# Kernel tuning notes

Hardware: AMD Instinct MI355X
Metric: run time of the kernel (lower is better)

## Reference

```python
import jax, jax.numpy as jnp
import numpy as np

M, N, K, T, BATCH = 1024, 128, 256, 10, 8192
LAMBD = 1.0


def setup_inputs() -> dict:
    key = jax.random.key(0)
    ks = jax.random.split(key, 4)
    y = jax.random.normal(ks[0], (BATCH, 2, N), dtype=jnp.float32)
    # xavier_normal scales, matching nn.init.xavier_normal_
    W = jax.random.normal(ks[1], (2, N, K), dtype=jnp.float32) * np.float32(np.sqrt(2.0 / (N + K)))
    WX = jax.random.normal(ks[2], (2, K, N), dtype=jnp.float32) * np.float32(np.sqrt(2.0 / (K + N)))
    E0 = jax.random.normal(ks[3], (2, M, K), dtype=jnp.float32) * np.float32(np.sqrt(2.0 / (M + K)))
    etas = jnp.full((T + 1, 1, 1), 1e-4, dtype=jnp.float32)   # original init 1e-4*ones
    gammas = jnp.ones((T + 1, 1, 1), dtype=jnp.float32)       # original init ones
    return {"y": y, "W": W, "WX": WX, "E0": E0, "etas": etas, "gammas": gammas}


def cmatmul(A, X):
    # complex matmul in 2-channel real form: A (2,p,q), X (2,q,B) -> (2,p,B)
    re = A[0] @ X[0] - A[1] @ X[1]
    im = A[0] @ X[1] + A[1] @ X[0]
    return jnp.stack([re, im])


def softshrink(z, lambd):
    return jnp.sign(z) * jnp.maximum(jnp.abs(z) - lambd, 0.0)


def huber(a, b):
    # F.smooth_l1_loss / huber with delta=1, mean reduction
    d = a - b
    ad = jnp.abs(d)
    return jnp.mean(jnp.where(ad < 1.0, 0.5 * d * d, ad - 0.5))


def reference(y, W, WX, E0, etas, gammas):
    B = y.shape[0]
    # complex_feature_transmission: (B,2,N) -> (2,B,N); then .transpose(1,2) -> (2,N,B)
    yt = jnp.transpose(y, (1, 2, 0))
    x = jnp.zeros((2, K, B), dtype=y.dtype)
    loss_sparse = jnp.float32(0.0)
    loss_eq = jnp.float32(0.0)
    xsp = jnp.zeros((2, M, B), dtype=y.dtype)
    for i in range(1, T + 1):
        # gradient step: x = x - gamma_i * WX (W x - y)
        x = x - gammas[i] * cmatmul(WX, cmatmul(W, x) - yt)
        # encode with shared EncodeW1[0]
        xsp = cmatmul(E0, x)  # (2,M,B)
        eta = etas[i]
        xsp = eta * softshrink(xsp / eta, LAMBD)
        # decoderW = conj(E0)^T; recovery uses only the real part xsp[0] (as in source)
        x_map = jnp.stack([E0[0].T @ xsp[0], -(E0[1].T) @ xsp[0]])  # (2,K,B)
        loss_sparse = loss_sparse + jnp.mean(jnp.sum(jnp.abs(xsp[0]), axis=0))
        loss_eq = loss_eq + huber(x, x_map)
        x = x_map
    x_T = jnp.transpose(x, (0, 2, 1))  # (2,B,K)
    xsp_T0 = jnp.transpose(xsp, (0, 2, 1))[0]  # (B,M)
    # sparse_degree: avg number of non-negligible coefficients per sample
    out_sparse = jnp.mean(jnp.sum((jnp.abs(xsp_T0) > 1e-3).astype(y.dtype), axis=1))
    return (x_T, loss_sparse, loss_eq / T, out_sparse)
```

## Files before the change

### kernel.cpp

```cpp
#include <hip/hip_runtime.h>
#include <stdint.h>


typedef short s8v __attribute__((ext_vector_type(8)));
typedef short s4v __attribute__((ext_vector_type(4)));
typedef float f16v __attribute__((ext_vector_type(16)));
typedef long long i64;

#define MFMA(a, b, c)  __builtin_amdgcn_mfma_f32_32x32x16_bf16((a), (b), (c), 0, 0, 0)
#define MFMA8(a, b, c) __builtin_amdgcn_mfma_f32_32x32x16_fp8_fp8((a), (b), (c), 0, 0, 0)

__device__ __forceinline__ short f2bf(float f) {
  uint32_t u = __builtin_bit_cast(uint32_t, f);
  u = (u + 0x7FFFu + ((u >> 16) & 1u)) >> 16;
  return (short)u;
}
__device__ __forceinline__ float bf2f(short s) {
  uint32_t u = ((uint32_t)(uint16_t)s) << 16;
  return __builtin_bit_cast(float, u);
}
__device__ __forceinline__ unsigned char f2fp8(float v) {
  return (unsigned char)(__builtin_amdgcn_cvt_pk_fp8_f32(v, 0.f, 0, false) & 0xFF);
}
__device__ __forceinline__ int pk4fp8(float a, float b, float c, float d) {
  int r = __builtin_amdgcn_cvt_pk_fp8_f32(a, b, 0, false);
  r = __builtin_amdgcn_cvt_pk_fp8_f32(c, d, r, true);
  return r;
}

__device__ __forceinline__ void glds16(const void* g, void* l) {
  __builtin_amdgcn_global_load_lds(
      (const __attribute__((address_space(1))) void*)g,
      (__attribute__((address_space(3))) void*)l, 16, 0, 0);
}
__device__ __forceinline__ void waitvm(int n) {
  if (n <= 0)      asm volatile("s_waitcnt vmcnt(0)" ::: "memory");
  else if (n == 2) asm volatile("s_waitcnt vmcnt(2)" ::: "memory");
  else             asm volatile("s_waitcnt vmcnt(4)" ::: "memory");
}


__global__ void prep_all(const float* __restrict__ W, const float* __restrict__ WX,
                         const float* __restrict__ E0,
                         short* __restrict__ Cbp, short* __restrict__ WXbp,
                         unsigned char* __restrict__ E0f8p,
                         unsigned char* __restrict__ E0Tf8p,
                         float* __restrict__ out) {
  const int b = blockIdx.x;
  if (b < 768) {
    const int idx = b * 256 + threadIdx.x;
    const int sec = idx >> 16, r = idx & 65535;
    const int j = r & 7, l31 = (r >> 3) & 31, h = (r >> 8) & 1, kc = (r >> 9) & 15, rt = r >> 13;
    const int i = rt * 32 + l31, col = kc * 16 + h * 8 + j;
    float c0 = 0.f, c1 = 0.f;
    for (int n = 0; n < 128; n++) {
      const float wx0 = WX[i * 128 + n], wx1 = WX[32768 + i * 128 + n];
      const float w0 = W[n * 256 + col], w1 = W[32768 + n * 256 + col];
      c0 += wx0 * w0 - wx1 * w1;
      c1 += wx0 * w1 + wx1 * w0;
    }
    Cbp[idx] = f2bf(sec == 0 ? c0 : (sec == 1 ? c1 : -c1));
  } else if (b < 1024) {
    const int idx = (b - 768) * 256 + threadIdx.x;
    const int sec = idx >> 15, r = idx & 32767;
    const int j = r & 7, l31 = (r >> 3) & 31, h = (r >> 8) & 1, kc = (r >> 9) & 7, rt = r >> 12;
    const int row = rt * 32 + l31, col = kc * 16 + h * 8 + j;
    WXbp[idx] = f2bf(-WX[sec * 32768 + row * 128 + col]);
  } else if (b < 3072) {
    const int idx = (b - 1024) * 256 + threadIdx.x;
    const int sec = idx >> 18, r = idx & 262143;
    const int blk = r >> 10, within = r & 1023;
    const int mt = blk >> 3, dkc = blk & 7;
    const int u = within >> 3, jj = within & 7;
    const int t = u >> 6, h = (u >> 5) & 1, l31 = u & 31;
    const int m = mt * 32 + l31, k = (dkc * 2 + t) * 16 + h * 8 + jj;
    const float v = E0[sec * 262144 + m * 256 + k] * (sec ? -16.f : 16.f);
    E0f8p[idx] = f2fp8(v);
  } else if (b < 5120) {
    const int idx = (b - 3072) * 256 + threadIdx.x;
    const int sec = idx >> 18, r = idx & 262143;
    const int blk = r >> 10, within = r & 1023;
    const int rt = blk >> 5, rem = blk & 31;
    const int c = rem >> 4, dkc = rem & 15;
    const int u = within >> 3, jj = within & 7;
    const int t = u >> 6, h = (u >> 5) & 1, l31 = u & 31;
    const int krow = rt * 32 + l31;
    const int mcol = c * 512 + (dkc * 2 + t) * 16 + h * 8 + jj;
    const float v = E0[sec * 262144 + mcol * 256 + krow] * (sec ? -16.f : 16.f);
    E0Tf8p[idx] = f2fp8(v);
  } else {
    if (threadIdx.x < 3) out[4194304 + threadIdx.x] = 0.f;
  }
}


#define RING(s) (((s) % 3) == 0 ? ring0 : ((s) % 3) == 1 ? ring1 : ring2)

__global__ __attribute__((amdgpu_flat_work_group_size(512, 512), amdgpu_waves_per_eu(2, 2)))
void ista_main(
    const float* __restrict__ y,
    const float* __restrict__ etas,
    const float* __restrict__ gammas,
    const short* __restrict__ Cbp,
    const short* __restrict__ WXbp,
    const unsigned char* __restrict__ E0f8p,
    const unsigned char* __restrict__ E0Tf8p,
    float* __restrict__ out) {
  __shared__ short buf0[16384];
  __shared__ short buf1[16384];
  __shared__ short bufy[12288];
  __shared__ unsigned char gxf8[16384];
  __shared__ unsigned char ring0[16384];
  __shared__ unsigned char ring1[16384];
  __shared__ unsigned char ring2[16384];
  unsigned char* zf8 = (unsigned char*)buf0;

  const int tid = threadIdx.x;
  const int w = tid >> 6;
  const int lane = tid & 63;
  const int l31 = lane & 31;
  const int h = lane >> 5;
  const int sw = l31 & 7;
  const int b0 = blockIdx.x * 32;
  const int lq = l31 * 8;
  const int lane16 = lane * 16;
  const int wslot = w * 2048;

  {
    const int bt = tid >> 4, j = tid & 15;
    const float* yb = y + (size_t)(b0 + bt) * 256;
    const int bsw = (bt & 7);
    #pragma unroll
    for (int rep = 0; rep < 2; rep++) {
      const int jj = j + rep * 16;
      const int ch = jj >> 4, n8 = (jj & 15) << 3;
      const float4 v0 = *(const float4*)(yb + ch * 128 + n8);
      const float4 v1 = *(const float4*)(yb + ch * 128 + n8 + 4);
      s8v pk;
      pk[0] = f2bf(v0.x); pk[1] = f2bf(v0.y); pk[2] = f2bf(v0.z); pk[3] = f2bf(v0.w);
      pk[4] = f2bf(v1.x); pk[5] = f2bf(v1.y); pk[6] = f2bf(v1.z); pk[7] = f2bf(v1.w);
      const int off = bt * 128 + (((n8 >> 3) ^ bsw) << 3);
      *(s8v*)(bufy + ch * 4096 + off) = pk;
      if (ch == 1) {
        s8v nk;
        #pragma unroll
        for (int e = 0; e < 8; e++) nk[e] = pk[e] ^ (short)0x8000;
        *(s8v*)(bufy + 8192 + off) = nk;
      }
    }
  }
  {
    s8v z = {0, 0, 0, 0, 0, 0, 0, 0};
    #pragma unroll
    for (int r = 0; r < 4; r++) *(s8v*)(buf0 + tid * 32 + r * 8) = z;
  }
  __syncthreads();

  float ls = 0.f, leq = 0.f, cntf = 0.f;
  float S = 1.f;
  float s16_last = 0.0625f;
  f16v xm0, xm1;
  #pragma unroll
  for (int r = 0; r < 16; r++) { xm0[r] = 0.f; xm1[r] = 0.f; }

  #pragma unroll 1
  for (int it = 1; it <= 10; it++) {
    const float gam = gammas[it];
    const float eta = etas[it];
    const float invS = 1.f / S;
    const float s16 = S * 0.0625f;
    s16_last = s16;

    f16v ac0, ac1;
    #pragma unroll
    for (int r = 0; r < 16; r++) { ac0[r] = 0.f; ac1[r] = 0.f; }
    #pragma unroll
    for (int kc = 0; kc < 8; kc++) {
      const int pa = ((w * 8 + kc) * 2 + h) * 256 + lq;
      const s8v a0 = *(const s8v*)(WXbp + pa);
      const s8v a1 = *(const s8v*)(WXbp + 32768 + pa);
      const int yo = l31 * 128 + ((((kc * 2 + h)) ^ sw) << 3);
      const s8v by0 = *(const s8v*)(bufy + yo);
      const s8v by1 = *(const s8v*)(bufy + 4096 + yo);
      const s8v by1n = *(const s8v*)(bufy + 8192 + yo);
      ac0 = MFMA(a0, by0, ac0);
      ac0 = MFMA(a1, by1n, ac0);
      ac1 = MFMA(a0, by1, ac1);
      ac1 = MFMA(a1, by0, ac1);
    }
    if (it > 1) {
      #pragma unroll
      for (int kc = 0; kc < 16; kc++) {
        const int pa = ((w * 16 + kc) * 2 + h) * 256 + lq;
        const s8v a0 = *(const s8v*)(Cbp + pa);
        const s8v a1 = *(const s8v*)(Cbp + 65536 + pa);
        const s8v a1n = *(const s8v*)(Cbp + 131072 + pa);
        const int xo = l31 * 256 + ((((kc * 2 + h)) ^ sw) << 3);
        const s8v bx0 = *(const s8v*)(buf0 + xo);
        const s8v bx1 = *(const s8v*)(buf0 + 8192 + xo);
        ac0 = MFMA(a0, bx0, ac0);
        ac0 = MFMA(a1n, bx1, ac0);
        ac1 = MFMA(a0, bx1, ac1);
        ac1 = MFMA(a1, bx0, ac1);
      }
    }
    #pragma unroll
    for (int r1 = 0; r1 < 4; r1++) {
      const int k0 = w * 32 + 8 * r1 + 4 * h;
      const int idx = l31 * 256 + (((k0 >> 3) ^ sw) << 3) + (k0 & 7);
      const s4v xv0 = *(const s4v*)(buf0 + idx);
      const s4v xv1 = *(const s4v*)(buf0 + 8192 + idx);
      float g0[4], g1[4];
      s4v p0, p1;
      #pragma unroll
      for (int r0 = 0; r0 < 4; r0++) {
        g0[r0] = bf2f(xv0[r0]) - gam * ac0[r1 * 4 + r0];
        g1[r0] = bf2f(xv1[r0]) - gam * ac1[r1 * 4 + r0];
        p0[r0] = f2bf(g0[r0]);
        p1[r0] = f2bf(g1[r0]);
      }
      *(s4v*)(buf1 + idx) = p0;
      *(s4v*)(buf1 + 8192 + idx) = p1;
      const int ga = l31 * 256 + (((k0 >> 4) ^ sw) << 4) + (k0 & 15);
      *(int*)(gxf8 + ga) = pk4fp8(g0[0] * invS, g0[1] * invS, g0[2] * invS, g0[3] * invS);
      *(int*)(gxf8 + 8192 + ga) = pk4fp8(g1[0] * invS, g1[1] * invS, g1[2] * invS, g1[3] * invS);
    }
    __syncthreads();

    #pragma unroll
    for (int r = 0; r < 16; r++) { xm0[r] = 0.f; xm1[r] = 0.f; }

    #pragma unroll 1
    for (int c = 0; c < 2; c++) {
      #pragma unroll 1
      for (int q = 0; q < 2; q++) {
        const int mt = c * 16 + q * 8 + w;
        const unsigned char* gb = E0f8p + (size_t)(mt * 8) * 1024 + lane16;
        f16v zq;
        #pragma unroll
        for (int r = 0; r < 16; r++) zq[r] = 0.f;

#define B_ISSUE(d) do { \
    unsigned char* _s = RING(d) + wslot; \
    glds16(gb + (d) * 1024, _s); \
    glds16(gb + 262144 + (d) * 1024, _s + 1024); \
  } while (0)

        B_ISSUE(0); B_ISSUE(1); B_ISSUE(2);
        #pragma unroll
        for (int dkc = 0; dkc < 8; dkc++) {
          waitvm(2 * (7 - dkc < 2 ? 7 - dkc : 2));
          const unsigned char* Sl = RING(dkc) + wslot;
          #pragma unroll
          for (int t = 0; t < 2; t++) {
            const i64 are = *(const i64*)(Sl + t * 512 + h * 256 + l31 * 8);
            const i64 aim = *(const i64*)(Sl + 1024 + t * 512 + h * 256 + l31 * 8);
            const int kc = dkc * 2 + t;
            const int go = l31 * 256 + ((kc ^ sw) << 4) + h * 8;
            const i64 bg0 = *(const i64*)(gxf8 + go);
            const i64 bg1 = *(const i64*)(gxf8 + 8192 + go);
            zq = MFMA8(are, bg0, zq);
            zq = MFMA8(aim, bg1, zq);
          }
          if (dkc + 3 < 8) B_ISSUE(dkc + 3);
        }
#undef B_ISSUE

        const int mtl = q * 8 + w;
        #pragma unroll
        for (int r1 = 0; r1 < 4; r1++) {
          float sv[4];
          #pragma unroll
          for (int r0 = 0; r0 < 4; r0++) {
            const float v = zq[r1 * 4 + r0] * s16;
            const float av = fabsf(v) - eta;
            float s = 0.f;
            if (av > 0.f) {
              s = (v > 0.f) ? av : -av;
              ls += av;
              if (it == 10 && av > 1e-3f) cntf += 1.f;
            }
            sv[r0] = s * invS;
          }
          const int ml = mtl * 32 + 8 * r1 + 4 * h;
          const int za = l31 * 512 + (((ml >> 4) ^ sw) << 4) + (ml & 15);
          *(int*)(zf8 + za) = pk4fp8(sv[0], sv[1], sv[2], sv[3]);
        }
      }
      __syncthreads();

      {
        const unsigned char* tb = E0Tf8p + (size_t)((w * 2 + c) * 16) * 1024 + lane16;
#define C_ISSUE(d) do { \
    unsigned char* _s = RING(d) + wslot; \
    glds16(tb + (d) * 1024, _s); \
    glds16(tb + 262144 + (d) * 1024, _s + 1024); \
  } while (0)

        C_ISSUE(0); C_ISSUE(1); C_ISSUE(2);
        #pragma unroll
        for (int dkc = 0; dkc < 16; dkc++) {
          waitvm(2 * (15 - dkc < 2 ? 15 - dkc : 2));
          const unsigned char* Sl = RING(dkc) + wslot;
          #pragma unroll
          for (int t = 0; t < 2; t++) {
            const i64 a0 = *(const i64*)(Sl + t * 512 + h * 256 + l31 * 8);
            const i64 a1 = *(const i64*)(Sl + 1024 + t * 512 + h * 256 + l31 * 8);
            const int kc = dkc * 2 + t;
            const i64 bz = *(const i64*)(zf8 + l31 * 512 + ((kc ^ sw) << 4) + h * 8);
            xm0 = MFMA8(a0, bz, xm0);
            xm1 = MFMA8(a1, bz, xm1);
          }
          if (dkc + 3 < 16) C_ISSUE(dkc + 3);
        }
#undef C_ISSUE
      }
      __syncthreads();
    }

    #pragma unroll
    for (int r1 = 0; r1 < 4; r1++) {
      const int k0 = w * 32 + 8 * r1 + 4 * h;
      const int idx = l31 * 256 + (((k0 >> 3) ^ sw) << 3) + (k0 & 7);
      const s4v gv0 = *(const s4v*)(buf1 + idx);
      const s4v gv1 = *(const s4v*)(buf1 + 8192 + idx);
      s4v p0, p1;
      #pragma unroll
      for (int r0 = 0; r0 < 4; r0++) {
        const float x0 = xm0[r1 * 4 + r0] * s16, x1 = xm1[r1 * 4 + r0] * s16;
        const float d0 = bf2f(gv0[r0]) - x0;
        const float d1 = bf2f(gv1[r0]) - x1;
        const float a0 = fabsf(d0), a1 = fabsf(d1);
        leq += (a0 < 1.f) ? 0.5f * d0 * d0 : (a0 - 0.5f);
        leq += (a1 < 1.f) ? 0.5f * d1 * d1 : (a1 - 0.5f);
        p0[r0] = f2bf(x0);
        p1[r0] = f2bf(x1);
      }
      *(s4v*)(buf0 + idx) = p0;
      *(s4v*)(buf0 + 8192 + idx) = p1;
    }
    __syncthreads();
    S *= 8.f;
  }

  {
    const size_t ob = (size_t)(b0 + l31) * 256;
    #pragma unroll
    for (int r1 = 0; r1 < 4; r1++) {
      const int k0 = w * 32 + 8 * r1 + 4 * h;
      float4 v0, v1;
      v0.x = xm0[r1 * 4 + 0] * s16_last; v0.y = xm0[r1 * 4 + 1] * s16_last;
      v0.z = xm0[r1 * 4 + 2] * s16_last; v0.w = xm0[r1 * 4 + 3] * s16_last;
      v1.x = xm1[r1 * 4 + 0] * s16_last; v1.y = xm1[r1 * 4 + 1] * s16_last;
      v1.z = xm1[r1 * 4 + 2] * s16_last; v1.w = xm1[r1 * 4 + 3] * s16_last;
      *(float4*)(out + ob + k0) = v0;
      *(float4*)(out + 2097152 + ob + k0) = v1;
    }
  }
  #pragma unroll
  for (int off = 32; off > 0; off >>= 1) {
    ls += __shfl_down(ls, off);
    leq += __shfl_down(leq, off);
    cntf += __shfl_down(cntf, off);
  }
  if (lane == 0) {
    atomicAdd(out + 4194304, ls * (1.f / 8192.f));
    atomicAdd(out + 4194305, leq * (1.f / (2.f * 256.f * 8192.f * 10.f)));
    atomicAdd(out + 4194306, cntf * (1.f / 8192.f));
  }
}

extern "C" void kernel_launch(void* const* d_in, const int* in_sizes, int n_in,
                              void* d_out, int out_size, void* d_ws, size_t ws_size,
                              hipStream_t stream) {
  (void)in_sizes; (void)n_in; (void)out_size; (void)ws_size;
  const float* y = (const float*)d_in[0];
  const float* W = (const float*)d_in[1];
  const float* WX = (const float*)d_in[2];
  const float* E0 = (const float*)d_in[3];
  const float* etas = (const float*)d_in[4];
  const float* gammas = (const float*)d_in[5];
  float* out = (float*)d_out;

  short* Cbp = (short*)d_ws;
  short* WXbp = Cbp + 196608;
  unsigned char* E0f8p = (unsigned char*)(WXbp + 65536);
  unsigned char* E0Tf8p = E0f8p + 524288;

  prep_all<<<5121, 256, 0, stream>>>(W, WX, E0, Cbp, WXbp, E0f8p, E0Tf8p, out);
  ista_main<<<256, 512, 0, stream>>>(y, etas, gammas, Cbp, WXbp, E0f8p, E0Tf8p, out);
}
```

Baseline: 441.7 us.

## Deepen LDS ring to five stages and prefetch across phases

Grows the global-to-LDS prefetch ring from three to five buffers with four loads in flight, and prefetches the first stages of the next matmul phase (next E0 tile or E0T tile) during the tail of the current loop so the pipeline does not drain at phase boundaries. The gradient-step intermediate is kept in registers instead of an LDS buffer, which frees shared memory for the extra ring slots. MFMA sections are wrapped in s_setprio to favour matrix issue. Risks include higher register pressure and fragile vmcnt bookkeeping, since cross-phase prefetches change how many loads are outstanding.

```diff
diff --git a/kernel.cpp b/kernel.cpp
--- a/kernel.cpp
+++ b/kernel.cpp
@@ -36,7 +36,8 @@
 __device__ __forceinline__ void waitvm(int n) {
   if (n <= 0)      asm volatile("s_waitcnt vmcnt(0)" ::: "memory");
   else if (n == 2) asm volatile("s_waitcnt vmcnt(2)" ::: "memory");
-  else             asm volatile("s_waitcnt vmcnt(4)" ::: "memory");
+  else if (n == 4) asm volatile("s_waitcnt vmcnt(4)" ::: "memory");
+  else             asm volatile("s_waitcnt vmcnt(6)" ::: "memory");
 }
 
 
@@ -94,7 +95,8 @@
 }
 
 
-#define RING(s) (((s) % 3) == 0 ? ring0 : ((s) % 3) == 1 ? ring1 : ring2)
+#define RING(s) (((s) % 5) == 0 ? ring0 : ((s) % 5) == 1 ? ring1 : \
+                 ((s) % 5) == 2 ? ring2 : ((s) % 5) == 3 ? ring3 : ring4)
 
 __global__ __attribute__((amdgpu_flat_work_group_size(512, 512), amdgpu_waves_per_eu(2, 2)))
 void ista_main(
@@ -107,12 +109,13 @@
     const unsigned char* __restrict__ E0Tf8p,
     float* __restrict__ out) {
   __shared__ short buf0[16384];
-  __shared__ short buf1[16384];
   __shared__ short bufy[12288];
   __shared__ unsigned char gxf8[16384];
   __shared__ unsigned char ring0[16384];
   __shared__ unsigned char ring1[16384];
   __shared__ unsigned char ring2[16384];
+  __shared__ unsigned char ring3[16384];
+  __shared__ unsigned char ring4[16384];
   unsigned char* zf8 = (unsigned char*)buf0;
 
   const int tid = threadIdx.x;
@@ -153,6 +156,15 @@
     s8v z = {0, 0, 0, 0, 0, 0, 0, 0};
     #pragma unroll
     for (int r = 0; r < 4; r++) *(s8v*)(buf0 + tid * 32 + r * 8) = z;
+  }
+  {
+    const unsigned char* gb0 = E0f8p + (size_t)(w * 8) * 1024 + lane16;
+    #pragma unroll
+    for (int d = 0; d < 3; d++) {
+      unsigned char* _s = RING(d) + wslot;
+      glds16(gb0 + d * 1024, _s);
+      glds16(gb0 + 262144 + d * 1024, _s + 1024);
+    }
   }
   __syncthreads();
 
@@ -204,6 +216,7 @@
         ac1 = MFMA(a1, bx0, ac1);
       }
     }
+    s4v gxr0[4], gxr1[4];
     #pragma unroll
     for (int r1 = 0; r1 < 4; r1++) {
       const int k0 = w * 32 + 8 * r1 + 4 * h;
@@ -219,8 +232,8 @@
         p0[r0] = f2bf(g0[r0]);
         p1[r0] = f2bf(g1[r0]);
       }
-      *(s4v*)(buf1 + idx) = p0;
-      *(s4v*)(buf1 + 8192 + idx) = p1;
+      gxr0[r1] = p0;
+      gxr1[r1] = p1;
       const int ga = l31 * 256 + (((k0 >> 4) ^ sw) << 4) + (k0 & 15);
       *(int*)(gxf8 + ga) = pk4fp8(g0[0] * invS, g0[1] * invS, g0[2] * invS, g0[3] * invS);
       *(int*)(gxf8 + 8192 + ga) = pk4fp8(g1[0] * invS, g1[1] * invS, g1[2] * invS, g1[3] * invS);
@@ -232,6 +245,8 @@
 
     #pragma unroll 1
     for (int c = 0; c < 2; c++) {
+      const unsigned char* tb = E0Tf8p + (size_t)((w * 2 + c) * 16) * 1024 + lane16;
+
       #pragma unroll 1
       for (int q = 0; q < 2; q++) {
         const int mt = c * 16 + q * 8 + w;
@@ -246,11 +261,12 @@
     glds16(gb + 262144 + (d) * 1024, _s + 1024); \
   } while (0)
 
-        B_ISSUE(0); B_ISSUE(1); B_ISSUE(2);
+        B_ISSUE(3);
         #pragma unroll
         for (int dkc = 0; dkc < 8; dkc++) {
-          waitvm(2 * (7 - dkc < 2 ? 7 - dkc : 2));
+          waitvm(dkc <= 4 ? 6 : 4);
           const unsigned char* Sl = RING(dkc) + wslot;
+          __builtin_amdgcn_s_setprio(1);
           #pragma unroll
           for (int t = 0; t < 2; t++) {
             const i64 are = *(const i64*)(Sl + t * 512 + h * 256 + l31 * 8);
@@ -262,7 +278,20 @@
             zq = MFMA8(are, bg0, zq);
             zq = MFMA8(aim, bg1, zq);
           }
-          if (dkc + 3 < 8) B_ISSUE(dkc + 3);
+          __builtin_amdgcn_s_setprio(0);
+          if (dkc + 4 < 8) {
+            B_ISSUE(dkc + 4);
+          } else {
+            const int j = dkc - 5;
+            unsigned char* _s = RING(j) + wslot;
+            if (q == 0) {
+              glds16(gb + 65536 + j * 1024, _s);
+              glds16(gb + 65536 + 262144 + j * 1024, _s + 1024);
+            } else {
+              glds16(tb + j * 1024, _s);
+              glds16(tb + 262144 + j * 1024, _s + 1024);
+            }
+          }
         }
 #undef B_ISSUE
 
@@ -290,18 +319,18 @@
       __syncthreads();
 
       {
-        const unsigned char* tb = E0Tf8p + (size_t)((w * 2 + c) * 16) * 1024 + lane16;
 #define C_ISSUE(d) do { \
     unsigned char* _s = RING(d) + wslot; \
     glds16(tb + (d) * 1024, _s); \
     glds16(tb + 262144 + (d) * 1024, _s + 1024); \
   } while (0)
 
-        C_ISSUE(0); C_ISSUE(1); C_ISSUE(2);
+        C_ISSUE(3);
         #pragma unroll
         for (int dkc = 0; dkc < 16; dkc++) {
-          waitvm(2 * (15 - dkc < 2 ? 15 - dkc : 2));
+          waitvm(dkc <= 12 ? 6 : dkc == 13 ? 4 : dkc == 14 ? 2 : 0);
           const unsigned char* Sl = RING(dkc) + wslot;
+          __builtin_amdgcn_s_setprio(1);
           #pragma unroll
           for (int t = 0; t < 2; t++) {
             const i64 a0 = *(const i64*)(Sl + t * 512 + h * 256 + l31 * 8);
@@ -311,9 +340,18 @@
             xm0 = MFMA8(a0, bz, xm0);
             xm1 = MFMA8(a1, bz, xm1);
           }
-          if (dkc + 3 < 16) C_ISSUE(dkc + 3);
+          __builtin_amdgcn_s_setprio(0);
+          if (dkc + 4 < 16) C_ISSUE(dkc + 4);
         }
 #undef C_ISSUE
+        const unsigned char* gbn =
+            E0f8p + (size_t)(((c == 0 ? 16 : 0) + w) * 8) * 1024 + lane16;
+        #pragma unroll
+        for (int j = 0; j < 3; j++) {
+          unsigned char* _s = RING(j) + wslot;
+          glds16(gbn + j * 1024, _s);
+          glds16(gbn + 262144 + j * 1024, _s + 1024);
+        }
       }
       __syncthreads();
     }
@@ -322,8 +360,8 @@
     for (int r1 = 0; r1 < 4; r1++) {
       const int k0 = w * 32 + 8 * r1 + 4 * h;
       const int idx = l31 * 256 + (((k0 >> 3) ^ sw) << 3) + (k0 & 7);
-      const s4v gv0 = *(const s4v*)(buf1 + idx);
-      const s4v gv1 = *(const s4v*)(buf1 + 8192 + idx);
+      const s4v gv0 = gxr0[r1];
+      const s4v gv1 = gxr1[r1];
       s4v p0, p1;
       #pragma unroll
       for (int r0 = 0; r0 < 4; r0++) {
```

Result: slower. 547.9 us (+24.0%).
